# Kernel optimization log

Measured on AMD Instinct MI355X. Metric: run time of the kernel, lower is better.

The kernel has to match this reference:

```python
import jax, jax.numpy as jnp
import numpy as np

NP_PEP, NP_PROT = 50000, 8000
E, EL = 1_600_000, 200_000
F_IN, H = 1280, 128


def _mean_aggr(x_src, src_idx, dst_idx, n_dst):
    # gather source feats per edge, scatter-mean into destination nodes
    msg = jax.ops.segment_sum(x_src[src_idx], dst_idx, num_segments=n_dst)  # [n_dst, H]
    deg = jax.ops.segment_sum(jnp.ones((src_idx.shape[0], 1), x_src.dtype), dst_idx, num_segments=n_dst)
    return msg / jnp.maximum(deg, 1.0)


def _hetero_sage(x_pep, x_prot, e_src, e_dst,
                 Wl_b, Wr_b, b_b, Wl_r, Wr_r, b_r):
    # edge type pep->prot (bind): updates prot nodes
    m_prot = _mean_aggr(x_pep, e_src, e_dst, x_prot.shape[0])
    out_prot = m_prot @ Wl_b + x_prot @ Wr_b + b_b
    # edge type prot->pep (rev_bind): updates pep nodes
    m_pep = _mean_aggr(x_prot, e_dst, e_src, x_pep.shape[0])
    out_pep = m_pep @ Wl_r + x_pep @ Wr_r + b_r
    return out_pep, out_prot


def setup_inputs() -> dict:
    key = jax.random.key(0)
    ks = jax.random.split(key, 24)
    s = 0.02
    inp = {
        'x_pep': jax.random.normal(ks[0], (NP_PEP, F_IN), jnp.float32),
        'x_prot': jax.random.normal(ks[1], (NP_PROT, F_IN), jnp.float32),
        'e_src': jax.random.randint(ks[2], (E,), 0, NP_PEP, jnp.int32),
        'e_dst': jax.random.randint(ks[3], (E,), 0, NP_PROT, jnp.int32),
        'el_src': jax.random.randint(ks[4], (EL,), 0, NP_PEP, jnp.int32),
        'el_dst': jax.random.randint(ks[5], (EL,), 0, NP_PROT, jnp.int32),
        'W_pep': s * jax.random.normal(ks[6], (F_IN, H), jnp.float32),
        'b_pep': jnp.zeros((H,), jnp.float32),
        'W_prot': s * jax.random.normal(ks[7], (F_IN, H), jnp.float32),
        'b_prot': jnp.zeros((H,), jnp.float32),
    }
    names = ['Wl1_bind', 'Wr1_bind', 'Wl1_rev', 'Wr1_rev',
             'Wl2_bind', 'Wr2_bind', 'Wl2_rev', 'Wr2_rev']
    for i, n in enumerate(names):
        inp[n] = s * jax.random.normal(ks[8 + i], (H, H), jnp.float32)
    for n in ['b1_bind', 'b1_rev', 'b2_bind', 'b2_rev']:
        inp[n] = jnp.zeros((H,), jnp.float32)
    return inp


def reference(x_pep, x_prot, e_src, e_dst, el_src, el_dst,
              W_pep, b_pep, W_prot, b_prot,
              Wl1_bind, Wr1_bind, b1_bind, Wl1_rev, Wr1_rev, b1_rev,
              Wl2_bind, Wr2_bind, b2_bind, Wl2_rev, Wr2_rev, b2_rev):
    # input projections (pep_emb/prot_emb unused in original forward)
    h_pep = x_pep @ W_pep + b_pep      # [NP_PEP, H]
    h_prot = x_prot @ W_prot + b_prot  # [NP_PROT, H]
    # SAGE layer 1 + relu
    h_pep, h_prot = _hetero_sage(h_pep, h_prot, e_src, e_dst,
                                 Wl1_bind, Wr1_bind, b1_bind,
                                 Wl1_rev, Wr1_rev, b1_rev)
    h_pep, h_prot = jax.nn.relu(h_pep), jax.nn.relu(h_prot)
    # SAGE layer 2
    h_pep, h_prot = _hetero_sage(h_pep, h_prot, e_src, e_dst,
                                 Wl2_bind, Wr2_bind, b2_bind,
                                 Wl2_rev, Wr2_rev, b2_rev)
    # classifier: edge-indexed gather + dot product
    return (h_pep[el_src] * h_prot[el_dst]).sum(axis=-1)  # [EL]
```

## Files before the change

kernel.cpp:

```cpp
#include <hip/hip_runtime.h>
#include <hip/hip_bf16.h>
#include <cstdint>

#define NP_PEP 50000
#define NP_PROT 8000
#define NE 1600000
#define NEL 200000
#define F_IN 1280
#define HDIM 128

#define CHUNK 4096
#define NBLK 391
#define NBQ 500
#define SHQ 4
#define NPBQ 16
#define NBP 391
#define SHP 7
#define NPBP 128

#define PROJ_BLK_PEP 391
#define PROJ_BLK_PROT 63
#define PROJ_TOT (PROJ_BLK_PEP + PROJ_BLK_PROT)
#define AGG_BLK_PROT 2000
#define AGG_BLK_PEP 12500

typedef __attribute__((ext_vector_type(8))) short bfrag;
typedef __attribute__((ext_vector_type(4))) short bhalf4;
typedef __attribute__((ext_vector_type(4))) float f32x4;

__device__ __forceinline__ ushort f2bf(float x) {
    __hip_bfloat16 h = __float2bfloat16(x);
    ushort u;
    __builtin_memcpy(&u, &h, 2);
    return u;
}
__device__ inline void unpack2(uint u, float& lo, float& hi) {
    union { uint u; float f; } a, b;
    a.u = u << 16; b.u = u & 0xffff0000u;
    lo = a.f; hi = b.f;
}
__device__ inline uint pack2(float a, float b) {
    return (uint)f2bf(a) | ((uint)f2bf(b) << 16);
}

__device__ __forceinline__ void cp16_g2l(const void* g, void* l) {
    __builtin_amdgcn_global_load_lds(
        (const __attribute__((address_space(1))) void*)g,
        (__attribute__((address_space(3))) void*)l, 16, 0, 0);
}

__device__ __forceinline__ int wscan_incl(int x) {
#pragma unroll
    for (int d = 1; d < 64; d <<= 1) {
        int y = __shfl_up(x, d);
        if ((int)(threadIdx.x & 63) >= d) x += y;
    }
    return x;
}

#define WST_TILE 4096

__global__ __launch_bounds__(512) void prep_count(const int* __restrict__ esrc,
                                                  const int* __restrict__ edst,
                                                  int* __restrict__ Gq,
                                                  int* __restrict__ Gp,
                                                  const float* __restrict__ Wp,
                                                  const float* __restrict__ Wq,
                                                  const float* __restrict__ m0,
                                                  const float* __restrict__ m1,
                                                  const float* __restrict__ m2,
                                                  const float* __restrict__ m3,
                                                  const float* __restrict__ m4,
                                                  const float* __restrict__ m5,
                                                  const float* __restrict__ m6,
                                                  const float* __restrict__ m7,
                                                  ushort* __restrict__ wout) {
    int b = blockIdx.x;
    if (b >= NBLK) {
        int bb = b - NBLK;
        const float* W; int kt; size_t base;
        if (bb < 40)      { W = Wp; kt = bb;       base = 0; }
        else if (bb < 80) { W = Wq; kt = bb - 40;  base = (size_t)40 * WST_TILE; }
        else {
            int mm = (bb - 80) >> 2; kt = (bb - 80) & 3;
            switch (mm) {
                case 0: W = m0; break; case 1: W = m1; break;
                case 2: W = m2; break; case 3: W = m3; break;
                case 4: W = m4; break; case 5: W = m5; break;
                case 6: W = m6; break; default: W = m7; break;
            }
            base = (size_t)(80 + 4 * mm) * WST_TILE;
        }
        int idx = threadIdx.x;
        int n = ((idx >> 6) << 4) | (idx & 15);
        int h = (idx >> 4) & 3;
        const float* wp = W + (size_t)(kt * 32 + h * 8) * HDIM + n;
        bfrag p;
#pragma unroll
        for (int j = 0; j < 8; ++j) p[j] = (short)f2bf(wp[(size_t)j * HDIM]);
        *(bfrag*)&wout[base + (size_t)kt * WST_TILE + (size_t)idx * 8] = p;
        return;
    }
    __shared__ int hq[NBQ];
    __shared__ int hp[NBP];
    int t = threadIdx.x;
    if (t < NBQ) hq[t] = 0;
    if (t < NBP) hp[t] = 0;
    __syncthreads();
    int e0 = b * CHUNK, cnt = min(CHUNK, NE - e0);
#pragma unroll
    for (int r = 0; r < 8; ++r) {
        int i = t + r * 512;
        if (i < cnt) {
            atomicAdd(&hq[edst[e0 + i] >> SHQ], 1);
            atomicAdd(&hp[esrc[e0 + i] >> SHP], 1);
        }
    }
    __syncthreads();
    if (t < NBQ) Gq[t * NBLK + b] = hq[t];
    if (t < NBP) Gp[t * NBLK + b] = hp[t];
}

__global__ __launch_bounds__(512) void rel_offsets(const int* __restrict__ Gq,
                                                   int* __restrict__ Oq, int* __restrict__ Tq,
                                                   const int* __restrict__ Gp,
                                                   int* __restrict__ Op, int* __restrict__ Tp) {
    const int* G; int* O; int* T; int j;
    if (blockIdx.x < NBQ) { G = Gq; O = Oq; T = Tq; j = blockIdx.x; }
    else                  { G = Gp; O = Op; T = Tp; j = blockIdx.x - NBQ; }
    __shared__ int wsum[8];
    int t = threadIdx.x;
    int lane = t & 63, wid = t >> 6;
    int v = (t < NBLK) ? G[j * NBLK + t] : 0;
    int inc = wscan_incl(v);
    if (lane == 63) wsum[wid] = inc;
    __syncthreads();
    int add = 0;
#pragma unroll
    for (int w = 0; w < 7; ++w)
        if (w < wid) add += wsum[w];
    inc += add;
    if (t < NBLK) O[j * NBLK + t] = inc - v;
    if (t == 511) T[j] = inc;
}

__global__ __launch_bounds__(512) void base_scan(const int* __restrict__ Tq, int* __restrict__ Bq,
                                                 const int* __restrict__ Tp, int* __restrict__ Bp) {
    __shared__ int wsum[8];
    int t = threadIdx.x;
    int lane = t & 63, wid = t >> 6;
    int v = (t < NBQ) ? Tq[t] : 0;
    int inc = wscan_incl(v);
    if (lane == 63) wsum[wid] = inc;
    __syncthreads();
    int add = 0;
#pragma unroll
    for (int w = 0; w < 7; ++w)
        if (w < wid) add += wsum[w];
    inc += add;
    if (t < NBQ) Bq[t] = inc - v;
    if (t == 0) Bq[NBQ] = NE;
    __syncthreads();
    int v2 = (t < NBP) ? Tp[t] : 0;
    int inc2 = wscan_incl(v2);
    if (lane == 63) wsum[wid] = inc2;
    __syncthreads();
    add = 0;
#pragma unroll
    for (int w = 0; w < 7; ++w)
        if (w < wid) add += wsum[w];
    inc2 += add;
    if (t < NBP) Bp[t] = inc2 - v2;
    if (t == 0) Bp[NBP] = NE;
}

__global__ __launch_bounds__(512) void bin_scatter2(const int* __restrict__ esrc,
                                                    const int* __restrict__ edst,
                                                    const int* __restrict__ Oq,
                                                    const int* __restrict__ Bq,
                                                    const int* __restrict__ Op,
                                                    const int* __restrict__ Bp,
                                                    uint* __restrict__ stagQ,
                                                    uint* __restrict__ stagP) {
    __shared__ int hist[512];
    __shared__ int start[512];
    __shared__ uint sorted[CHUNK];
    __shared__ int wsum[8];
    int b = blockIdx.x, t = threadIdx.x;
    int lane = t & 63, wid = t >> 6;
    int e0 = b * CHUNK, cnt = min(CHUNK, NE - e0);
    uint pk[8];
    bool val[8];
#pragma unroll
    for (int r = 0; r < 8; ++r) {
        int i = t + r * 512;
        val[r] = (i < cnt);
        if (val[r]) {
            int s = esrc[e0 + i], d = edst[e0 + i];
            pk[r] = ((uint)s << 13) | (uint)d;
        }
    }
    for (int dir = 0; dir < 2; ++dir) {
        const int* O = dir ? Op : Oq;
        const int* B = dir ? Bp : Bq;
        uint* stg = dir ? stagP : stagQ;
        int shf = dir ? SHP : SHQ;
        hist[t] = 0;
        __syncthreads();
        int bk[8];
#pragma unroll
        for (int r = 0; r < 8; ++r) {
            bk[r] = -1;
            if (val[r]) {
                int key = dir ? (int)(pk[r] >> 13) : (int)(pk[r] & 8191u);
                bk[r] = key >> shf;
                atomicAdd(&hist[bk[r]], 1);
            }
        }
        __syncthreads();
        int ownv = hist[t];
        int inc = wscan_incl(ownv);
        if (lane == 63) wsum[wid] = inc;
        __syncthreads();
        int add = 0;
#pragma unroll
        for (int w = 0; w < 7; ++w)
            if (w < wid) add += wsum[w];
        int excl = inc + add - ownv;
        start[t] = excl;
        hist[t] = excl;
        __syncthreads();
#pragma unroll
        for (int r = 0; r < 8; ++r)
            if (bk[r] >= 0) {
                int rank = atomicAdd(&hist[bk[r]], 1);
                sorted[rank] = pk[r];
            }
        __syncthreads();
#pragma unroll
        for (int r = 0; r < 8; ++r) {
            int i = t + r * 512;
            if (i < cnt) {
                uint v = sorted[i];
                int key = dir ? (int)(v >> 13) : (int)(v & 8191u);
                int bb = key >> shf;
                stg[B[bb] + O[bb * NBLK + b] + (i - start[bb])] = v;
            }
        }
        __syncthreads();
    }
}

__global__ __launch_bounds__(256) void proj_fincsr(
    const float* __restrict__ Aa, const ushort* __restrict__ Wsta,
    const float* __restrict__ ba, ushort* __restrict__ Ca, int Ma,
    const float* __restrict__ Ab, const ushort* __restrict__ Wstb,
    const float* __restrict__ bb_, ushort* __restrict__ Cb, int Mb,
    const uint* __restrict__ stagQ, const int* __restrict__ Bq,
    int* __restrict__ rowptr_prot, int* __restrict__ col_prot,
    const uint* __restrict__ stagP, const int* __restrict__ Bp,
    int* __restrict__ rowptr_pep, int* __restrict__ col_pep) {
    __shared__ ushort Alds[4096];
    __shared__ ushort Blds[4096];
    __shared__ ushort Clds[128 * 136];
    int bx = blockIdx.x;
    int tid = threadIdx.x;
    if (bx < PROJ_TOT) {
        const float* A; const ushort* Wst; const float* bias; ushort* Cg; int M, blk;
        if (bx < PROJ_BLK_PEP) { A = Aa; Wst = Wsta; bias = ba; Cg = Ca; M = Ma; blk = bx; }
        else                   { A = Ab; Wst = Wstb; bias = bb_; Cg = Cb; M = Mb; blk = bx - PROJ_BLK_PEP; }
        int lane = tid & 63, w = tid >> 6, wm = w >> 1, wn = w & 1;
        int r0 = blk * 128;

        f32x4 acc[4][4];
#pragma unroll
        for (int i = 0; i < 4; ++i)
#pragma unroll
            for (int j = 0; j < 4; ++j) acc[i][j] = (f32x4){0.f, 0.f, 0.f, 0.f};

        for (int kt = 0; kt < F_IN / 32; ++kt) {
            int k0 = kt * 32;
            const ushort* wsrc = Wst + (size_t)kt * WST_TILE;
            cp16_g2l(wsrc + (size_t)tid * 8, &Blds[(size_t)tid * 8]);
            cp16_g2l(wsrc + 2048 + (size_t)tid * 8, &Blds[2048 + (size_t)tid * 8]);
#pragma unroll
            for (int i = 0; i < 4; ++i) {
                int idx = tid + 256 * i;
                int row = idx >> 3, q = idx & 7;
                int gr = min(r0 + row, M - 1);
                float4 v = *(const float4*)(A + (size_t)gr * F_IN + k0 + q * 4);
                bhalf4 p;
                p.x = (short)f2bf(v.x); p.y = (short)f2bf(v.y);
                p.z = (short)f2bf(v.z); p.w = (short)f2bf(v.w);
                int off = ((row >> 4) * 64 + ((q >> 1) << 4) + (row & 15)) * 8 + (q & 1) * 4;
                *(bhalf4*)&Alds[off] = p;
            }
            __syncthreads();
            const bfrag* Af = (const bfrag*)Alds;
            const bfrag* Bf = (const bfrag*)Blds;
            bfrag af[4], bf_[4];
#pragma unroll
            for (int i = 0; i < 4; ++i) af[i] = Af[(wm * 4 + i) * 64 + lane];
#pragma unroll
            for (int j = 0; j < 4; ++j) bf_[j] = Bf[(wn * 4 + j) * 64 + lane];
#pragma unroll
            for (int i = 0; i < 4; ++i)
#pragma unroll
                for (int j = 0; j < 4; ++j)
                    acc[i][j] = __builtin_amdgcn_mfma_f32_16x16x32_bf16(af[i], bf_[j], acc[i][j], 0, 0, 0);
            __syncthreads();
        }
#pragma unroll
        for (int j = 0; j < 4; ++j) {
            int colL = wn * 64 + j * 16 + (lane & 15);
            float bcol = bias[colL];
#pragma unroll
            for (int i = 0; i < 4; ++i) {
                int rbase = wm * 64 + i * 16 + ((lane >> 4) << 2);
                f32x4 v = acc[i][j];
                Clds[(rbase + 0) * 136 + colL] = f2bf(v.x + bcol);
                Clds[(rbase + 1) * 136 + colL] = f2bf(v.y + bcol);
                Clds[(rbase + 2) * 136 + colL] = f2bf(v.z + bcol);
                Clds[(rbase + 3) * 136 + colL] = f2bf(v.w + bcol);
            }
        }
        __syncthreads();
#pragma unroll
        for (int c = 0; c < 8; ++c) {
            int cidx = c * 256 + tid;
            int row = cidx >> 4, h = cidx & 15;
            int gr = r0 + row;
            if (gr < M)
                *(bfrag*)(Cg + (size_t)gr * HDIM + h * 8) = *(const bfrag*)&Clds[row * 136 + h * 8];
        }
        return;
    }
    int fb = bx - PROJ_TOT;
    int* cnts = (int*)Alds;
    int* cur  = cnts + 128;
    int* wsf  = cur + 128;
    const uint* stg; const int* B; int* rowptr; int* col;
    int n, npb, j, use_dst;
    if (fb < NBQ) {
        stg = stagQ; B = Bq; rowptr = rowptr_prot; col = col_prot;
        n = NP_PROT; npb = NPBQ; j = fb; use_dst = 1;
    } else {
        stg = stagP; B = Bp; rowptr = rowptr_pep; col = col_pep;
        n = NP_PEP; npb = NPBP; j = fb - NBQ; use_dst = 0;
    }
    int t = tid;
    int first = j * npb;
    int nn = min(npb, n - first);
    if (t < 128) cnts[t] = 0;
    __syncthreads();
    int s0 = B[j], s1 = B[j + 1];
    for (int i = s0 + t; i < s1; i += 256) {
        uint v = stg[i];
        int key = use_dst ? (int)(v & 8191u) : (int)(v >> 13);
        atomicAdd(&cnts[key - first], 1);
    }
    __syncthreads();
    int v = (t < 128) ? cnts[t] : 0;
    int inc = wscan_incl(v);
    if (t == 63) wsf[0] = inc;
    __syncthreads();
    if (t >= 64 && t < 128) inc += wsf[0];
    if (t < 128) {
        int excl = inc - v;
        if (t < nn) rowptr[first + t] = s0 + excl;
        cur[t] = s0 + excl;
    }
    if (t == 0 && j == 0) rowptr[n] = NE;
    __syncthreads();
    for (int i = s0 + t; i < s1; i += 256) {
        uint v2 = stg[i];
        int key, pay;
        if (use_dst) { key = (int)(v2 & 8191u); pay = (int)(v2 >> 13); }
        else         { key = (int)(v2 >> 13);   pay = (int)(v2 & 8191u); }
        int pos = atomicAdd(&cur[key - first], 1);
        col[pos] = pay;
    }
}

__global__ __launch_bounds__(256) void lin2f(const ushort* A1a, const ushort* W1a,
                                             const ushort* A2a, const ushort* W2a,
                                             const float* __restrict__ ba,
                                             ushort* Ca, int Ma, int nblk_a,
                                             const ushort* A1b, const ushort* W1b,
                                             const ushort* A2b, const ushort* W2b,
                                             const float* __restrict__ bb,
                                             ushort* Cb, int Mb, int do_relu) {
    __shared__ ushort Alds[4096];
    __shared__ ushort Blds[4096];
    __shared__ ushort Clds[128 * 136];
    const ushort *A1, *A2, *W1, *W2; const float* bias; ushort* C; int M, blk;
    if ((int)blockIdx.x < nblk_a) {
        A1 = A1a; W1 = W1a; A2 = A2a; W2 = W2a; bias = ba; C = Ca; M = Ma; blk = blockIdx.x;
    } else {
        A1 = A1b; W1 = W1b; A2 = A2b; W2 = W2b; bias = bb; C = Cb; M = Mb; blk = blockIdx.x - nblk_a;
    }
    int tid = threadIdx.x;
    int lane = tid & 63, w = tid >> 6, wm = w >> 1, wn = w & 1;
    int r0 = blk * 128;

    int arow = ((tid >> 6) << 4) | (tid & 15);
    int ah = (tid >> 4) & 3;
    int gr1 = min(r0 + arow, M - 1);
    int gr2 = min(r0 + arow + 64, M - 1);

    f32x4 acc[4][4];
#pragma unroll
    for (int i = 0; i < 4; ++i)
#pragma unroll
        for (int j = 0; j < 4; ++j) acc[i][j] = (f32x4){0.f, 0.f, 0.f, 0.f};

    for (int kt = 0; kt < 8; ++kt) {
        const ushort* A = (kt < 4) ? A1 : A2;
        const ushort* Wt = (kt < 4) ? W1 : W2;
        int k0 = (kt & 3) * 32;
        cp16_g2l(A + (size_t)gr1 * HDIM + k0 + ah * 8, &Alds[(size_t)tid * 8]);
        cp16_g2l(A + (size_t)gr2 * HDIM + k0 + ah * 8, &Alds[(size_t)(tid + 256) * 8]);
        const ushort* wsrc = Wt + (size_t)(kt & 3) * WST_TILE;
        cp16_g2l(wsrc + (size_t)tid * 8, &Blds[(size_t)tid * 8]);
        cp16_g2l(wsrc + 2048 + (size_t)tid * 8, &Blds[2048 + (size_t)tid * 8]);
        __syncthreads();
        const bfrag* Af = (const bfrag*)Alds;
        const bfrag* Bf = (const bfrag*)Blds;
        bfrag af[4], bf_[4];
#pragma unroll
        for (int i = 0; i < 4; ++i) af[i] = Af[(wm * 4 + i) * 64 + lane];
#pragma unroll
        for (int j = 0; j < 4; ++j) bf_[j] = Bf[(wn * 4 + j) * 64 + lane];
#pragma unroll
        for (int i = 0; i < 4; ++i)
#pragma unroll
            for (int j = 0; j < 4; ++j)
                acc[i][j] = __builtin_amdgcn_mfma_f32_16x16x32_bf16(af[i], bf_[j], acc[i][j], 0, 0, 0);
        __syncthreads();
    }
#pragma unroll
    for (int j = 0; j < 4; ++j) {
        int colL = wn * 64 + j * 16 + (lane & 15);
        float bcol = bias[colL];
#pragma unroll
        for (int i = 0; i < 4; ++i) {
            int rbase = wm * 64 + i * 16 + ((lane >> 4) << 2);
            f32x4 v = acc[i][j];
            float o0 = v.x + bcol, o1 = v.y + bcol, o2 = v.z + bcol, o3 = v.w + bcol;
            if (do_relu) {
                o0 = fmaxf(o0, 0.f); o1 = fmaxf(o1, 0.f);
                o2 = fmaxf(o2, 0.f); o3 = fmaxf(o3, 0.f);
            }
            Clds[(rbase + 0) * 136 + colL] = f2bf(o0);
            Clds[(rbase + 1) * 136 + colL] = f2bf(o1);
            Clds[(rbase + 2) * 136 + colL] = f2bf(o2);
            Clds[(rbase + 3) * 136 + colL] = f2bf(o3);
        }
    }
    __syncthreads();
#pragma unroll
    for (int c = 0; c < 8; ++c) {
        int cidx = c * 256 + tid;
        int row = cidx >> 4, h = cidx & 15;
        int gr = r0 + row;
        if (gr < M)
            *(bfrag*)(C + (size_t)gr * HDIM + h * 8) = *(const bfrag*)&Clds[row * 136 + h * 8];
    }
}

__global__ __launch_bounds__(256) void aggr2(const ushort* __restrict__ Ha,
                                             const int* __restrict__ rpa,
                                             const int* __restrict__ cola,
                                             ushort* __restrict__ Oa, int Na, int nblk_a,
                                             const ushort* __restrict__ Hb,
                                             const int* __restrict__ rpb,
                                             const int* __restrict__ colb,
                                             ushort* __restrict__ Ob, int Nb) {
    const ushort* H; const int* rp; const int* col; ushort* O; int N, blk;
    if ((int)blockIdx.x < nblk_a) { H = Ha; rp = rpa; col = cola; O = Oa; N = Na; blk = blockIdx.x; }
    else                          { H = Hb; rp = rpb; col = colb; O = Ob; N = Nb; blk = blockIdx.x - nblk_a; }
    int node = blk * 4 + (threadIdx.x >> 6);
    if (node >= N) return;
    int lane = threadIdx.x & 63;
    int sub = lane >> 4;
    int ch = lane & 15;
    int beg = rp[node], end = rp[node + 1];
    int deg = end - beg;
    float a0 = 0, a1 = 0, a2 = 0, a3 = 0, a4 = 0, a5 = 0, a6 = 0, a7 = 0;
    int j = beg + sub;
    for (; j + 12 < end; j += 16) {
        int i0 = col[j], i1 = col[j + 4], i2 = col[j + 8], i3 = col[j + 12];
        uint4 u0 = *(const uint4*)(H + (size_t)i0 * HDIM + ch * 8);
        uint4 u1 = *(const uint4*)(H + (size_t)i1 * HDIM + ch * 8);
        uint4 u2 = *(const uint4*)(H + (size_t)i2 * HDIM + ch * 8);
        uint4 u3 = *(const uint4*)(H + (size_t)i3 * HDIM + ch * 8);
        float lo, hi;
        unpack2(u0.x, lo, hi); a0 += lo; a1 += hi;
        unpack2(u0.y, lo, hi); a2 += lo; a3 += hi;
        unpack2(u0.z, lo, hi); a4 += lo; a5 += hi;
        unpack2(u0.w, lo, hi); a6 += lo; a7 += hi;
        unpack2(u1.x, lo, hi); a0 += lo; a1 += hi;
        unpack2(u1.y, lo, hi); a2 += lo; a3 += hi;
        unpack2(u1.z, lo, hi); a4 += lo; a5 += hi;
        unpack2(u1.w, lo, hi); a6 += lo; a7 += hi;
        unpack2(u2.x, lo, hi); a0 += lo; a1 += hi;
        unpack2(u2.y, lo, hi); a2 += lo; a3 += hi;
        unpack2(u2.z, lo, hi); a4 += lo; a5 += hi;
        unpack2(u2.w, lo, hi); a6 += lo; a7 += hi;
        unpack2(u3.x, lo, hi); a0 += lo; a1 += hi;
        unpack2(u3.y, lo, hi); a2 += lo; a3 += hi;
        unpack2(u3.z, lo, hi); a4 += lo; a5 += hi;
        unpack2(u3.w, lo, hi); a6 += lo; a7 += hi;
    }
    for (; j + 4 < end; j += 8) {
        int i0 = col[j], i1 = col[j + 4];
        uint4 u0 = *(const uint4*)(H + (size_t)i0 * HDIM + ch * 8);
        uint4 u1 = *(const uint4*)(H + (size_t)i1 * HDIM + ch * 8);
        float lo, hi;
        unpack2(u0.x, lo, hi); a0 += lo; a1 += hi;
        unpack2(u0.y, lo, hi); a2 += lo; a3 += hi;
        unpack2(u0.z, lo, hi); a4 += lo; a5 += hi;
        unpack2(u0.w, lo, hi); a6 += lo; a7 += hi;
        unpack2(u1.x, lo, hi); a0 += lo; a1 += hi;
        unpack2(u1.y, lo, hi); a2 += lo; a3 += hi;
        unpack2(u1.z, lo, hi); a4 += lo; a5 += hi;
        unpack2(u1.w, lo, hi); a6 += lo; a7 += hi;
    }
    if (j < end) {
        int i0 = col[j];
        uint4 u0 = *(const uint4*)(H + (size_t)i0 * HDIM + ch * 8);
        float lo, hi;
        unpack2(u0.x, lo, hi); a0 += lo; a1 += hi;
        unpack2(u0.y, lo, hi); a2 += lo; a3 += hi;
        unpack2(u0.z, lo, hi); a4 += lo; a5 += hi;
        unpack2(u0.w, lo, hi); a6 += lo; a7 += hi;
    }
    a0 += __shfl_xor(a0, 16); a0 += __shfl_xor(a0, 32);
    a1 += __shfl_xor(a1, 16); a1 += __shfl_xor(a1, 32);
    a2 += __shfl_xor(a2, 16); a2 += __shfl_xor(a2, 32);
    a3 += __shfl_xor(a3, 16); a3 += __shfl_xor(a3, 32);
    a4 += __shfl_xor(a4, 16); a4 += __shfl_xor(a4, 32);
    a5 += __shfl_xor(a5, 16); a5 += __shfl_xor(a5, 32);
    a6 += __shfl_xor(a6, 16); a6 += __shfl_xor(a6, 32);
    a7 += __shfl_xor(a7, 16); a7 += __shfl_xor(a7, 32);
    if (sub == 0) {
        float inv = 1.0f / (float)max(deg, 1);
        uint4 o;
        o.x = pack2(a0 * inv, a1 * inv);
        o.y = pack2(a2 * inv, a3 * inv);
        o.z = pack2(a4 * inv, a5 * inv);
        o.w = pack2(a6 * inv, a7 * inv);
        *(uint4*)(O + (size_t)node * HDIM + ch * 8) = o;
    }
}

__global__ __launch_bounds__(256) void classify_bf16(const ushort* __restrict__ hp,
                                                     const ushort* __restrict__ hr,
                                                     const int* __restrict__ esrc,
                                                     const int* __restrict__ edst,
                                                     float* __restrict__ out, int n) {
    int t = blockIdx.x * blockDim.x + threadIdx.x;
    int edge = t >> 4;
    int ch = t & 15;
    if (edge >= n) return;
    int s = esrc[edge], d = edst[edge];
    uint4 ua = *(const uint4*)(hp + (size_t)s * HDIM + ch * 8);
    uint4 ub = *(const uint4*)(hr + (size_t)d * HDIM + ch * 8);
    float al, ah, bl, bh;
    float v = 0.f;
    unpack2(ua.x, al, ah); unpack2(ub.x, bl, bh); v += al * bl + ah * bh;
    unpack2(ua.y, al, ah); unpack2(ub.y, bl, bh); v += al * bl + ah * bh;
    unpack2(ua.z, al, ah); unpack2(ub.z, bl, bh); v += al * bl + ah * bh;
    unpack2(ua.w, al, ah); unpack2(ub.w, bl, bh); v += al * bl + ah * bh;
    v += __shfl_xor(v, 8);
    v += __shfl_xor(v, 4);
    v += __shfl_xor(v, 2);
    v += __shfl_xor(v, 1);
    if (ch == 0) out[edge] = v;
}


extern "C" void kernel_launch(void* const* d_in, const int* in_sizes, int n_in,
                              void* d_out, int out_size, void* d_ws, size_t ws_size,
                              hipStream_t stream) {
    const float* x_pep   = (const float*)d_in[0];
    const float* x_prot  = (const float*)d_in[1];
    const int*   e_src   = (const int*)d_in[2];
    const int*   e_dst   = (const int*)d_in[3];
    const int*   el_src  = (const int*)d_in[4];
    const int*   el_dst  = (const int*)d_in[5];
    const float* W_pep   = (const float*)d_in[6];
    const float* b_pep   = (const float*)d_in[7];
    const float* W_prot  = (const float*)d_in[8];
    const float* b_prot  = (const float*)d_in[9];
    const float* Wl1_bind = (const float*)d_in[10];
    const float* Wr1_bind = (const float*)d_in[11];
    const float* Wl1_rev  = (const float*)d_in[12];
    const float* Wr1_rev  = (const float*)d_in[13];
    const float* Wl2_bind = (const float*)d_in[14];
    const float* Wr2_bind = (const float*)d_in[15];
    const float* Wl2_rev  = (const float*)d_in[16];
    const float* Wr2_rev  = (const float*)d_in[17];
    const float* b1_bind  = (const float*)d_in[18];
    const float* b1_rev   = (const float*)d_in[19];
    const float* b2_bind  = (const float*)d_in[20];
    const float* b2_rev   = (const float*)d_in[21];
    float* out = (float*)d_out;

    ushort* P0 = (ushort*)d_ws;
    ushort* P1 = P0 + (size_t)NP_PEP * HDIM;
    ushort* R0 = P1 + (size_t)NP_PEP * HDIM;
    ushort* R1 = R0 + (size_t)NP_PROT * HDIM;
    int* rowptr_pep  = (int*)(R1 + (size_t)NP_PROT * HDIM);
    int* rowptr_prot = rowptr_pep + NP_PEP + 1;
    int* col_pep     = rowptr_prot + NP_PROT + 1;
    int* col_prot    = col_pep + NE;
    uint* stagP      = (uint*)(col_prot + NE);
    uint* stagQ      = stagP + NE;
    int* Gq          = (int*)(stagQ + NE);
    int* Oq          = Gq + NBQ * NBLK;
    int* Gp          = Oq + NBQ * NBLK;
    int* Op          = Gp + NBP * NBLK;
    int* Tq          = Op + NBP * NBLK;
    int* Tp          = Tq + NBQ;
    int* Bq          = Tp + NBP;
    int* Bp          = Bq + NBQ + 1;
    uintptr_t wraw   = (uintptr_t)(Bp + NBP + 1);
    ushort* Wst      = (ushort*)((wraw + 255) & ~(uintptr_t)255);

    const ushort* WstPep  = Wst;
    const ushort* WstProt = Wst + (size_t)40 * WST_TILE;
    const ushort* WstL1b  = Wst + (size_t)(80 + 0)  * WST_TILE;
    const ushort* WstR1b  = Wst + (size_t)(80 + 4)  * WST_TILE;
    const ushort* WstL1r  = Wst + (size_t)(80 + 8)  * WST_TILE;
    const ushort* WstR1r  = Wst + (size_t)(80 + 12) * WST_TILE;
    const ushort* WstL2b  = Wst + (size_t)(80 + 16) * WST_TILE;
    const ushort* WstR2b  = Wst + (size_t)(80 + 20) * WST_TILE;
    const ushort* WstL2r  = Wst + (size_t)(80 + 24) * WST_TILE;
    const ushort* WstR2r  = Wst + (size_t)(80 + 28) * WST_TILE;

    prep_count<<<NBLK + 112, 512, 0, stream>>>(e_src, e_dst, Gq, Gp,
                                               W_pep, W_prot,
                                               Wl1_bind, Wr1_bind, Wl1_rev, Wr1_rev,
                                               Wl2_bind, Wr2_bind, Wl2_rev, Wr2_rev, Wst);
    rel_offsets<<<NBQ + NBP, 512, 0, stream>>>(Gq, Oq, Tq, Gp, Op, Tp);
    base_scan<<<1, 512, 0, stream>>>(Tq, Bq, Tp, Bp);
    bin_scatter2<<<NBLK, 512, 0, stream>>>(e_src, e_dst, Oq, Bq, Op, Bp, stagQ, stagP);

    proj_fincsr<<<PROJ_TOT + NBQ + NBP, 256, 0, stream>>>(
        x_pep, WstPep, b_pep, P0, NP_PEP,
        x_prot, WstProt, b_prot, R0, NP_PROT,
        stagQ, Bq, rowptr_prot, col_prot,
        stagP, Bp, rowptr_pep, col_pep);

    aggr2<<<AGG_BLK_PROT + AGG_BLK_PEP, 256, 0, stream>>>(
        P0, rowptr_prot, col_prot, R1, NP_PROT, AGG_BLK_PROT,
        R0, rowptr_pep, col_pep, P1, NP_PEP);
    lin2f<<<PROJ_BLK_PEP + PROJ_BLK_PROT, 256, 0, stream>>>(
        P1, WstL1r, P0, WstR1r, b1_rev, P1, NP_PEP, PROJ_BLK_PEP,
        R1, WstL1b, R0, WstR1b, b1_bind, R1, NP_PROT, 1);

    aggr2<<<AGG_BLK_PROT + AGG_BLK_PEP, 256, 0, stream>>>(
        P1, rowptr_prot, col_prot, R0, NP_PROT, AGG_BLK_PROT,
        R1, rowptr_pep, col_pep, P0, NP_PEP);
    lin2f<<<PROJ_BLK_PEP + PROJ_BLK_PROT, 256, 0, stream>>>(
        P0, WstL2r, P1, WstR2r, b2_rev, P0, NP_PEP, PROJ_BLK_PEP,
        R0, WstL2b, R1, WstR2b, b2_bind, R0, NP_PROT, 0);

    classify_bf16<<<(NEL * 16 + 255) / 256, 256, 0, stream>>>(P0, R0, el_src, el_dst, out, NEL);
}
```

Baseline: 636.3 us.

## Restructure CSR build pipeline: fuse base scan, overlap scatter with projection

Folds the single-block base scan into the relative-offset kernel using a last-block ticket counter, which removes one launch. The bin scatter now runs inside the same kernel as the input projection, so the scatter overlaps with the MFMA GEMM. The projection moves to 512-thread blocks with a 4x2 wave layout. CSR finalization becomes its own kernel that stages column indices in shared memory as ushort before writing them out coalesced. This trades an extra launch for finalize against better overlap. It also risks ticket-ordering subtleties and truncation, since pep indices above 65535 cannot fit in a ushort, though here they are under 8192 or 50000.

```diff
diff --git a/kernel.cpp b/kernel.cpp
--- a/kernel.cpp
+++ b/kernel.cpp
@@ -23,6 +23,8 @@
 #define PROJ_TOT (PROJ_BLK_PEP + PROJ_BLK_PROT)
 #define AGG_BLK_PROT 2000
 #define AGG_BLK_PEP 12500
+
+#define FIN_CAP 5120
 
 typedef __attribute__((ext_vector_type(8))) short bfrag;
 typedef __attribute__((ext_vector_type(4))) short bhalf4;
@@ -74,10 +76,12 @@
                                                   const float* __restrict__ m5,
                                                   const float* __restrict__ m6,
                                                   const float* __restrict__ m7,
-                                                  ushort* __restrict__ wout) {
+                                                  ushort* __restrict__ wout,
+                                                  int* __restrict__ ticket) {
     int b = blockIdx.x;
     if (b >= NBLK) {
         int bb = b - NBLK;
+        if (bb == 0 && threadIdx.x == 0) *ticket = 0;
         const float* W; int kt; size_t base;
         if (bb < 40)      { W = Wp; kt = bb;       base = 0; }
         else if (bb < 80) { W = Wq; kt = bb - 40;  base = (size_t)40 * WST_TILE; }
@@ -121,14 +125,17 @@
     if (t < NBP) Gp[t * NBLK + b] = hp[t];
 }
 
-__global__ __launch_bounds__(512) void rel_offsets(const int* __restrict__ Gq,
-                                                   int* __restrict__ Oq, int* __restrict__ Tq,
-                                                   const int* __restrict__ Gp,
-                                                   int* __restrict__ Op, int* __restrict__ Tp) {
+__global__ __launch_bounds__(512) void rel_offsets_base(const int* __restrict__ Gq,
+                                                        int* __restrict__ Oq, int* __restrict__ Tq,
+                                                        const int* __restrict__ Gp,
+                                                        int* __restrict__ Op, int* __restrict__ Tp,
+                                                        int* __restrict__ Bq, int* __restrict__ Bp,
+                                                        int* __restrict__ ticket) {
     const int* G; int* O; int* T; int j;
     if (blockIdx.x < NBQ) { G = Gq; O = Oq; T = Tq; j = blockIdx.x; }
     else                  { G = Gp; O = Op; T = Tp; j = blockIdx.x - NBQ; }
     __shared__ int wsum[8];
+    __shared__ int lastflag;
     int t = threadIdx.x;
     int lane = t & 63, wid = t >> 6;
     int v = (t < NBLK) ? G[j * NBLK + t] : 0;
@@ -142,150 +149,75 @@
     inc += add;
     if (t < NBLK) O[j * NBLK + t] = inc - v;
     if (t == 511) T[j] = inc;
-}
-
-__global__ __launch_bounds__(512) void base_scan(const int* __restrict__ Tq, int* __restrict__ Bq,
-                                                 const int* __restrict__ Tp, int* __restrict__ Bp) {
-    __shared__ int wsum[8];
-    int t = threadIdx.x;
-    int lane = t & 63, wid = t >> 6;
-    int v = (t < NBQ) ? Tq[t] : 0;
-    int inc = wscan_incl(v);
-    if (lane == 63) wsum[wid] = inc;
-    __syncthreads();
-    int add = 0;
+    __syncthreads();
+    if (t == 0) {
+        __threadfence();
+        int done = atomicAdd(ticket, 1);
+        lastflag = (done == NBQ + NBP - 1) ? 1 : 0;
+    }
+    __syncthreads();
+    if (!lastflag) return;
+    __threadfence();
+    int v1 = (t < NBQ) ? Tq[t] : 0;
+    int i1 = wscan_incl(v1);
+    if (lane == 63) wsum[wid] = i1;
+    __syncthreads();
+    add = 0;
 #pragma unroll
     for (int w = 0; w < 7; ++w)
         if (w < wid) add += wsum[w];
-    inc += add;
-    if (t < NBQ) Bq[t] = inc - v;
+    i1 += add;
+    if (t < NBQ) Bq[t] = i1 - v1;
     if (t == 0) Bq[NBQ] = NE;
     __syncthreads();
     int v2 = (t < NBP) ? Tp[t] : 0;
-    int inc2 = wscan_incl(v2);
-    if (lane == 63) wsum[wid] = inc2;
+    int i2 = wscan_incl(v2);
+    if (lane == 63) wsum[wid] = i2;
     __syncthreads();
     add = 0;
 #pragma unroll
     for (int w = 0; w < 7; ++w)
         if (w < wid) add += wsum[w];
-    inc2 += add;
-    if (t < NBP) Bp[t] = inc2 - v2;
+    i2 += add;
+    if (t < NBP) Bp[t] = i2 - v2;
     if (t == 0) Bp[NBP] = NE;
 }
 
-__global__ __launch_bounds__(512) void bin_scatter2(const int* __restrict__ esrc,
-                                                    const int* __restrict__ edst,
-                                                    const int* __restrict__ Oq,
-                                                    const int* __restrict__ Bq,
-                                                    const int* __restrict__ Op,
-                                                    const int* __restrict__ Bp,
-                                                    uint* __restrict__ stagQ,
-                                                    uint* __restrict__ stagP) {
-    __shared__ int hist[512];
-    __shared__ int start[512];
-    __shared__ uint sorted[CHUNK];
-    __shared__ int wsum[8];
-    int b = blockIdx.x, t = threadIdx.x;
-    int lane = t & 63, wid = t >> 6;
-    int e0 = b * CHUNK, cnt = min(CHUNK, NE - e0);
-    uint pk[8];
-    bool val[8];
-#pragma unroll
-    for (int r = 0; r < 8; ++r) {
-        int i = t + r * 512;
-        val[r] = (i < cnt);
-        if (val[r]) {
-            int s = esrc[e0 + i], d = edst[e0 + i];
-            pk[r] = ((uint)s << 13) | (uint)d;
-        }
-    }
-    for (int dir = 0; dir < 2; ++dir) {
-        const int* O = dir ? Op : Oq;
-        const int* B = dir ? Bp : Bq;
-        uint* stg = dir ? stagP : stagQ;
-        int shf = dir ? SHP : SHQ;
-        hist[t] = 0;
-        __syncthreads();
-        int bk[8];
-#pragma unroll
-        for (int r = 0; r < 8; ++r) {
-            bk[r] = -1;
-            if (val[r]) {
-                int key = dir ? (int)(pk[r] >> 13) : (int)(pk[r] & 8191u);
-                bk[r] = key >> shf;
-                atomicAdd(&hist[bk[r]], 1);
-            }
-        }
-        __syncthreads();
-        int ownv = hist[t];
-        int inc = wscan_incl(ownv);
-        if (lane == 63) wsum[wid] = inc;
-        __syncthreads();
-        int add = 0;
-#pragma unroll
-        for (int w = 0; w < 7; ++w)
-            if (w < wid) add += wsum[w];
-        int excl = inc + add - ownv;
-        start[t] = excl;
-        hist[t] = excl;
-        __syncthreads();
-#pragma unroll
-        for (int r = 0; r < 8; ++r)
-            if (bk[r] >= 0) {
-                int rank = atomicAdd(&hist[bk[r]], 1);
-                sorted[rank] = pk[r];
-            }
-        __syncthreads();
-#pragma unroll
-        for (int r = 0; r < 8; ++r) {
-            int i = t + r * 512;
-            if (i < cnt) {
-                uint v = sorted[i];
-                int key = dir ? (int)(v >> 13) : (int)(v & 8191u);
-                int bb = key >> shf;
-                stg[B[bb] + O[bb * NBLK + b] + (i - start[bb])] = v;
-            }
-        }
-        __syncthreads();
-    }
-}
-
-__global__ __launch_bounds__(256) void proj_fincsr(
+__global__ __launch_bounds__(512) void scatter_proj(
     const float* __restrict__ Aa, const ushort* __restrict__ Wsta,
     const float* __restrict__ ba, ushort* __restrict__ Ca, int Ma,
     const float* __restrict__ Ab, const ushort* __restrict__ Wstb,
     const float* __restrict__ bb_, ushort* __restrict__ Cb, int Mb,
-    const uint* __restrict__ stagQ, const int* __restrict__ Bq,
-    int* __restrict__ rowptr_prot, int* __restrict__ col_prot,
-    const uint* __restrict__ stagP, const int* __restrict__ Bp,
-    int* __restrict__ rowptr_pep, int* __restrict__ col_pep) {
-    __shared__ ushort Alds[4096];
-    __shared__ ushort Blds[4096];
-    __shared__ ushort Clds[128 * 136];
+    const int* __restrict__ esrc, const int* __restrict__ edst,
+    const int* __restrict__ Oq, const int* __restrict__ Bq,
+    const int* __restrict__ Op, const int* __restrict__ Bp,
+    uint* __restrict__ stagQ, uint* __restrict__ stagP) {
+    __shared__ __align__(16) char smem[51200];
     int bx = blockIdx.x;
     int tid = threadIdx.x;
     if (bx < PROJ_TOT) {
+        ushort* Alds = (ushort*)smem;
+        ushort* Blds = Alds + 4096;
+        ushort* Clds = Blds + 4096;
         const float* A; const ushort* Wst; const float* bias; ushort* Cg; int M, blk;
         if (bx < PROJ_BLK_PEP) { A = Aa; Wst = Wsta; bias = ba; Cg = Ca; M = Ma; blk = bx; }
         else                   { A = Ab; Wst = Wstb; bias = bb_; Cg = Cb; M = Mb; blk = bx - PROJ_BLK_PEP; }
-        int lane = tid & 63, w = tid >> 6, wm = w >> 1, wn = w & 1;
+        int lane = tid & 63, w = tid >> 6, wm = w >> 2, wn = w & 3;
         int r0 = blk * 128;
 
-        f32x4 acc[4][4];
+        f32x4 acc[4][2];
 #pragma unroll
         for (int i = 0; i < 4; ++i)
 #pragma unroll
-            for (int j = 0; j < 4; ++j) acc[i][j] = (f32x4){0.f, 0.f, 0.f, 0.f};
+            for (int j = 0; j < 2; ++j) acc[i][j] = (f32x4){0.f, 0.f, 0.f, 0.f};
 
         for (int kt = 0; kt < F_IN / 32; ++kt) {
             int k0 = kt * 32;
             const ushort* wsrc = Wst + (size_t)kt * WST_TILE;
             cp16_g2l(wsrc + (size_t)tid * 8, &Blds[(size_t)tid * 8]);
-            cp16_g2l(wsrc + 2048 + (size_t)tid * 8, &Blds[2048 + (size_t)tid * 8]);
-#pragma unroll
-            for (int i = 0; i < 4; ++i) {
-                int idx = tid + 256 * i;
+#pragma unroll
+            for (int i = 0; i < 2; ++i) {
+                int idx = tid + 512 * i;
                 int row = idx >> 3, q = idx & 7;
                 int gr = min(r0 + row, M - 1);
                 float4 v = *(const float4*)(A + (size_t)gr * F_IN + k0 + q * 4);
@@ -298,21 +230,21 @@
             __syncthreads();
             const bfrag* Af = (const bfrag*)Alds;
             const bfrag* Bf = (const bfrag*)Blds;
-            bfrag af[4], bf_[4];
+            bfrag af[4], bf_[2];
 #pragma unroll
             for (int i = 0; i < 4; ++i) af[i] = Af[(wm * 4 + i) * 64 + lane];
 #pragma unroll
-            for (int j = 0; j < 4; ++j) bf_[j] = Bf[(wn * 4 + j) * 64 + lane];
+            for (int j = 0; j < 2; ++j) bf_[j] = Bf[(wn * 2 + j) * 64 + lane];
 #pragma unroll
             for (int i = 0; i < 4; ++i)
 #pragma unroll
-                for (int j = 0; j < 4; ++j)
+                for (int j = 0; j < 2; ++j)
                     acc[i][j] = __builtin_amdgcn_mfma_f32_16x16x32_bf16(af[i], bf_[j], acc[i][j], 0, 0, 0);
             __syncthreads();
         }
 #pragma unroll
-        for (int j = 0; j < 4; ++j) {
-            int colL = wn * 64 + j * 16 + (lane & 15);
+        for (int j = 0; j < 2; ++j) {
+            int colL = (wn * 2 + j) * 16 + (lane & 15);
             float bcol = bias[colL];
 #pragma unroll
             for (int i = 0; i < 4; ++i) {
@@ -326,8 +258,8 @@
         }
         __syncthreads();
 #pragma unroll
-        for (int c = 0; c < 8; ++c) {
-            int cidx = c * 256 + tid;
+        for (int c = 0; c < 4; ++c) {
+            int cidx = c * 512 + tid;
             int row = cidx >> 4, h = cidx & 15;
             int gr = r0 + row;
             if (gr < M)
@@ -335,25 +267,103 @@
         }
         return;
     }
-    int fb = bx - PROJ_TOT;
-    int* cnts = (int*)Alds;
-    int* cur  = cnts + 128;
-    int* wsf  = cur + 128;
+    int* hist   = (int*)smem;
+    int* start_ = hist + 512;
+    uint* sorted = (uint*)(start_ + 512);
+    int* wsum   = (int*)(sorted + CHUNK);
+    int b = bx - PROJ_TOT, t = tid;
+    int lane = t & 63, wid = t >> 6;
+    int e0 = b * CHUNK, cnt = min(CHUNK, NE - e0);
+    uint pk[8];
+    bool val[8];
+#pragma unroll
+    for (int r = 0; r < 8; ++r) {
+        int i = t + r * 512;
+        val[r] = (i < cnt);
+        if (val[r]) {
+            int s = esrc[e0 + i], d = edst[e0 + i];
+            pk[r] = ((uint)s << 13) | (uint)d;
+        }
+    }
+    for (int dir = 0; dir < 2; ++dir) {
+        const int* O = dir ? Op : Oq;
+        const int* B = dir ? Bp : Bq;
+        uint* stg = dir ? stagP : stagQ;
+        int shf = dir ? SHP : SHQ;
+        hist[t] = 0;
+        __syncthreads();
+        int bk[8];
+#pragma unroll
+        for (int r = 0; r < 8; ++r) {
+            bk[r] = -1;
+            if (val[r]) {
+                int key = dir ? (int)(pk[r] >> 13) : (int)(pk[r] & 8191u);
+                bk[r] = key >> shf;
+                atomicAdd(&hist[bk[r]], 1);
+            }
+        }
+        __syncthreads();
+        int ownv = hist[t];
+        int inc = wscan_incl(ownv);
+        if (lane == 63) wsum[wid] = inc;
+        __syncthreads();
+        int add = 0;
+#pragma unroll
+        for (int w = 0; w < 7; ++w)
+            if (w < wid) add += wsum[w];
+        int excl = inc + add - ownv;
+        start_[t] = excl;
+        hist[t] = excl;
+        __syncthreads();
+#pragma unroll
+        for (int r = 0; r < 8; ++r)
+            if (bk[r] >= 0) {
+                int rank = atomicAdd(&hist[bk[r]], 1);
+                sorted[rank] = pk[r];
+            }
+        __syncthreads();
+#pragma unroll
+        for (int r = 0; r < 8; ++r) {
+            int i = t + r * 512;
+            if (i < cnt) {
+                uint v = sorted[i];
+                int key = dir ? (int)(v >> 13) : (int)(v & 8191u);
+                int bb = key >> shf;
+                stg[B[bb] + O[bb * NBLK + b] + (i - start_[bb])] = v;
+            }
+        }
+        __syncthreads();
+    }
+}
+
+__global__ __launch_bounds__(256) void finalize_csr(const uint* __restrict__ stagQ,
+                                                    const int* __restrict__ Bq,
+                                                    int* __restrict__ rowptr_prot,
+                                                    int* __restrict__ col_prot,
+                                                    const uint* __restrict__ stagP,
+                                                    const int* __restrict__ Bp,
+                                                    int* __restrict__ rowptr_pep,
+                                                    int* __restrict__ col_pep) {
+    __shared__ int cnts[128];
+    __shared__ int cur[128];
+    __shared__ int wsf;
+    __shared__ ushort us[FIN_CAP];
     const uint* stg; const int* B; int* rowptr; int* col;
     int n, npb, j, use_dst;
-    if (fb < NBQ) {
+    if (blockIdx.x < NBQ) {
         stg = stagQ; B = Bq; rowptr = rowptr_prot; col = col_prot;
-        n = NP_PROT; npb = NPBQ; j = fb; use_dst = 1;
+        n = NP_PROT; npb = NPBQ; j = blockIdx.x; use_dst = 1;
     } else {
         stg = stagP; B = Bp; rowptr = rowptr_pep; col = col_pep;
-        n = NP_PEP; npb = NPBP; j = fb - NBQ; use_dst = 0;
-    }
-    int t = tid;
+        n = NP_PEP; npb = NPBP; j = blockIdx.x - NBQ; use_dst = 0;
+    }
+    int t = threadIdx.x;
     int first = j * npb;
     int nn = min(npb, n - first);
     if (t < 128) cnts[t] = 0;
     __syncthreads();
     int s0 = B[j], s1 = B[j + 1];
+    int cnt = s1 - s0;
     for (int i = s0 + t; i < s1; i += 256) {
         uint v = stg[i];
         int key = use_dst ? (int)(v & 8191u) : (int)(v >> 13);
@@ -362,23 +372,36 @@
     __syncthreads();
     int v = (t < 128) ? cnts[t] : 0;
     int inc = wscan_incl(v);
-    if (t == 63) wsf[0] = inc;
-    __syncthreads();
-    if (t >= 64 && t < 128) inc += wsf[0];
+    if (t == 63) wsf = inc;
+    __syncthreads();
+    if (t >= 64 && t < 128) inc += wsf;
     if (t < 128) {
         int excl = inc - v;
         if (t < nn) rowptr[first + t] = s0 + excl;
-        cur[t] = s0 + excl;
+        cur[t] = excl;
     }
     if (t == 0 && j == 0) rowptr[n] = NE;
     __syncthreads();
-    for (int i = s0 + t; i < s1; i += 256) {
-        uint v2 = stg[i];
-        int key, pay;
-        if (use_dst) { key = (int)(v2 & 8191u); pay = (int)(v2 >> 13); }
-        else         { key = (int)(v2 >> 13);   pay = (int)(v2 & 8191u); }
-        int pos = atomicAdd(&cur[key - first], 1);
-        col[pos] = pay;
+    if (cnt <= FIN_CAP) {
+        for (int i = s0 + t; i < s1; i += 256) {
+            uint v2 = stg[i];
+            int key, pay;
+            if (use_dst) { key = (int)(v2 & 8191u); pay = (int)(v2 >> 13); }
+            else         { key = (int)(v2 >> 13);   pay = (int)(v2 & 8191u); }
+            int pos = atomicAdd(&cur[key - first], 1);
+            us[pos] = (ushort)pay;
+        }
+        __syncthreads();
+        for (int i = t; i < cnt; i += 256) col[s0 + i] = (int)us[i];
+    } else {
+        for (int i = s0 + t; i < s1; i += 256) {
+            uint v2 = stg[i];
+            int key, pay;
+            if (use_dst) { key = (int)(v2 & 8191u); pay = (int)(v2 >> 13); }
+            else         { key = (int)(v2 >> 13);   pay = (int)(v2 & 8191u); }
+            int pos = atomicAdd(&cur[key - first], 1);
+            col[s0 + pos] = pay;
+        }
     }
 }
 
@@ -625,7 +648,8 @@
     int* Tp          = Tq + NBQ;
     int* Bq          = Tp + NBP;
     int* Bp          = Bq + NBQ + 1;
-    uintptr_t wraw   = (uintptr_t)(Bp + NBP + 1);
+    int* ticket      = Bp + NBP + 1;
+    uintptr_t wraw   = (uintptr_t)(ticket + 1);
     ushort* Wst      = (ushort*)((wraw + 255) & ~(uintptr_t)255);
 
     const ushort* WstPep  = Wst;
@@ -642,16 +666,17 @@
     prep_count<<<NBLK + 112, 512, 0, stream>>>(e_src, e_dst, Gq, Gp,
                                                W_pep, W_prot,
                                                Wl1_bind, Wr1_bind, Wl1_rev, Wr1_rev,
-                                               Wl2_bind, Wr2_bind, Wl2_rev, Wr2_rev, Wst);
-    rel_offsets<<<NBQ + NBP, 512, 0, stream>>>(Gq, Oq, Tq, Gp, Op, Tp);
-    base_scan<<<1, 512, 0, stream>>>(Tq, Bq, Tp, Bp);
-    bin_scatter2<<<NBLK, 512, 0, stream>>>(e_src, e_dst, Oq, Bq, Op, Bp, stagQ, stagP);
-
-    proj_fincsr<<<PROJ_TOT + NBQ + NBP, 256, 0, stream>>>(
+                                               Wl2_bind, Wr2_bind, Wl2_rev, Wr2_rev, Wst,
+                                               ticket);
+    rel_offsets_base<<<NBQ + NBP, 512, 0, stream>>>(Gq, Oq, Tq, Gp, Op, Tp, Bq, Bp, ticket);
+
+    scatter_proj<<<PROJ_TOT + NBLK, 512, 0, stream>>>(
         x_pep, WstPep, b_pep, P0, NP_PEP,
         x_prot, WstProt, b_prot, R0, NP_PROT,
-        stagQ, Bq, rowptr_prot, col_prot,
-        stagP, Bp, rowptr_pep, col_pep);
+        e_src, e_dst, Oq, Bq, Op, Bp, stagQ, stagP);
+
+    finalize_csr<<<NBQ + NBP, 256, 0, stream>>>(stagQ, Bq, rowptr_prot, col_prot,
+                                                stagP, Bp, rowptr_pep, col_pep);
 
     aggr2<<<AGG_BLK_PROT + AGG_BLK_PEP, 256, 0, stream>>>(
         P0, rowptr_prot, col_prot, R1, NP_PROT, AGG_BLK_PROT,
```

Result: slower. 660.8 us (+3.8%).
